# Optimization experiments

Hardware: AMD Instinct MI355X
Metric: run time of the kernel (lower is better)

The kernel has to match this reference:

```python
import jax, jax.numpy as jnp
from jax import lax
import numpy as np


def _qlayer(x, theta):
    """Simulate QLayer: RX(x_i) encoder + trainable RX(theta_i) per wire
    (they commute -> single RX(x_i+theta_i) on |0>), then ring of CNOTs,
    then <Z> on each wire.  x: (B, n) float, theta: (n,). Returns (B, n)."""
    B, n = x.shape
    a = x + theta[None, :]
    c = jnp.cos(a * 0.5)
    s = jnp.sin(a * 0.5)
    # RX(a)|0> = [cos(a/2), -i sin(a/2)] per wire -> product state
    amps = jnp.stack([c + 0j, -1j * s], axis=-1)  # (B, n, 2) complex64
    state = amps[:, 0]  # (B, 2)
    for w in range(1, n):
        state = state[..., None] * amps[:, w].reshape((B,) + (1,) * w + (2,))
    # state: (B, 2, 2, ..., 2), axis w+1 == wire w
    for ctrl in range(n):
        tgt = (ctrl + 1) % n
        s0 = jnp.take(state, 0, axis=ctrl + 1)   # control = 0 block
        s1 = jnp.take(state, 1, axis=ctrl + 1)   # control = 1 block
        t_ax = tgt + 1 if tgt < ctrl else tgt    # target axis after removing ctrl axis
        s1 = jnp.flip(s1, axis=t_ax)             # X on target
        state = jnp.stack([s0, s1], axis=ctrl + 1)
    p = state.real ** 2 + state.imag ** 2
    axes = tuple(range(1, n + 1))
    zs = []
    for w in range(n):
        other = tuple(ax for ax in axes if ax != w + 1)
        pw = jnp.sum(p, axis=other)              # (B, 2)
        zs.append(pw[:, 0] - pw[:, 1])           # <Z_w> = P(0) - P(1)
    return jnp.stack(zs, axis=1)


def setup_inputs() -> dict:
    key = jax.random.key(0)
    ks = jax.random.split(key, 13)
    T, B, D, NQ = 64, 256, 512, 6
    lim = 1.0 / np.sqrt(D + NQ)

    def lin(k):
        k1, k2 = jax.random.split(k)
        W = jax.random.uniform(k1, (D + NQ, NQ), jnp.float32, -lim, lim)
        b = jax.random.uniform(k2, (NQ,), jnp.float32, -lim, lim)
        return W, b

    Wf, bf = lin(ks[0]); Wi, bi = lin(ks[1]); Wu, bu = lin(ks[2]); Wo, bo = lin(ks[3])
    theta_f = jax.random.normal(ks[4], (NQ,), jnp.float32) * 0.1
    theta_i = jax.random.normal(ks[5], (NQ,), jnp.float32) * 0.1
    theta_u = jax.random.normal(ks[6], (NQ,), jnp.float32) * 0.1
    theta_o = jax.random.normal(ks[7], (NQ,), jnp.float32) * 0.1
    inputs = jax.random.normal(ks[8], (T, B, D), jnp.float32)
    return {"inputs": inputs,
            "Wf": Wf, "bf": bf, "Wi": Wi, "bi": bi,
            "Wu": Wu, "bu": bu, "Wo": Wo, "bo": bo,
            "theta_f": theta_f, "theta_i": theta_i,
            "theta_u": theta_u, "theta_o": theta_o}


def reference(inputs, Wf, bf, Wi, bi, Wu, bu, Wo, bo,
              theta_f, theta_i, theta_u, theta_o):
    B = inputs.shape[1]
    NQ = theta_f.shape[0]  # hidden_dim == n_qubits
    h0 = jnp.zeros((B, NQ), inputs.dtype)
    c0 = jnp.zeros((B, NQ), inputs.dtype)

    def step(carry, x):
        hx, cx = carry
        comb = jnp.concatenate([x, hx], axis=1)          # (B, D+NQ)
        f = jax.nn.sigmoid(_qlayer(comb @ Wf + bf, theta_f))
        i = jax.nn.sigmoid(_qlayer(comb @ Wi + bi, theta_i))
        g = jnp.tanh(_qlayer(comb @ Wu + bu, theta_u))
        o = jax.nn.sigmoid(_qlayer(comb @ Wo + bo, theta_o))
        cx2 = f * cx + i * g
        hx2 = o * jnp.tanh(cx2)
        return (hx2, cx2), hx2

    (hx, cx), outputs = lax.scan(step, (h0, c0), inputs)  # outputs: (T, B, NQ)
    return outputs, hx, cx
```

## Files before the change

kernel.cpp:

```cpp
#include <hip/hip_runtime.h>


typedef float v2f __attribute__((ext_vector_type(2)));

__device__ __forceinline__ float fast_rcp(float x) { return __builtin_amdgcn_rcpf(x); }

template <int CTRL>
__device__ __forceinline__ float dpp_add(float x) {
    int t = __builtin_amdgcn_mov_dpp(__float_as_int(x), CTRL, 0xF, 0xF, true);
    return x + __int_as_float(t);
}

template <int G>
__device__ __forceinline__ float quad_bcast(float v) {
    int i = __builtin_amdgcn_mov_dpp(__float_as_int(v), G * 0x55, 0xF, 0xF, true);
    return __int_as_float(i);
}

__global__ __launch_bounds__(512, 2) void gemm_pre(
    const float* __restrict__ X,
    const float* __restrict__ Wf, const float* __restrict__ bf,
    const float* __restrict__ Wi, const float* __restrict__ bi,
    const float* __restrict__ Wu, const float* __restrict__ bu,
    const float* __restrict__ Wo, const float* __restrict__ bo,
    const float* __restrict__ thf, const float* __restrict__ thi,
    const float* __restrict__ thu, const float* __restrict__ tho,
    float* __restrict__ pre)
{
    __shared__ float W_lds[13312];

    const int tid  = threadIdx.x;
    const int w    = tid >> 6;
    const int lane = tid & 63;
    const int rowbase = blockIdx.x * 64;

    #pragma unroll
    for (int i = 0; i < 4; ++i) {
        const float* Wp = (i==0)?Wf:(i==1)?Wi:(i==2)?Wu:Wo;
        int k = tid;
        const float2* s = (const float2*)(Wp + k*6);
        float2* d = (float2*)(W_lds + k*26 + i*6);
        d[0] = s[0]; d[1] = s[1]; d[2] = s[2];
    }
    __syncthreads();

    v2f acc[8][12];
    #pragma unroll
    for (int r = 0; r < 8; ++r)
        #pragma unroll
        for (int p = 0; p < 12; ++p) acc[r][p] = (v2f){0.f, 0.f};

    const float* Xr0 = X + (rowbase + w*8)*512 + lane;

    float pa[8];
    #pragma unroll
    for (int r = 0; r < 8; ++r) pa[r] = Xr0[r*512];

    #pragma unroll
    for (int kb = 0; kb < 512; kb += 64) {
        const v2f* wrow = (const v2f*)(W_lds + (kb + lane)*26);
        #pragma unroll
        for (int p = 0; p < 12; ++p) {
            v2f wv = wrow[p];
            #pragma unroll
            for (int r = 0; r < 8; ++r)
                acc[r][p] = __builtin_elementwise_fma((v2f){pa[r],pa[r]}, wv, acc[r][p]);
        }
        if (kb < 448) {
            #pragma unroll
            for (int r = 0; r < 8; ++r) pa[r] = Xr0[kb + 64 + r*512];
        }
    }

    #pragma unroll
    for (int r = 0; r < 8; ++r)
        #pragma unroll
        for (int p = 0; p < 12; ++p) {
            float x = acc[r][p].x;
            x = dpp_add<0xB1>(x);
            x = dpp_add<0x4E>(x);
            acc[r][p].x = x;
            float y = acc[r][p].y;
            y = dpp_add<0xB1>(y);
            y = dpp_add<0x4E>(y);
            acc[r][p].y = y;
        }

    #define ACCV(v) ((((v) & 1) == 0) ? acc[(v)/24][((v)%24)/2].x \
                                      : acc[(v)/24][((v)%24)/2].y)
    const int j = lane & 3;
    const int q = lane >> 2;
    const bool j1 = (j & 1) != 0, j2 = (j & 2) != 0;

    __syncthreads();

    #pragma unroll
    for (int pass = 0; pass < 2; ++pass) {
        if ((w >> 2) == pass) {
            const int w4 = w & 3;
            #pragma unroll
            for (int i = 0; i < 48; ++i) {
                float c0 = ACCV(i*4 + 0), c1 = ACCV(i*4 + 1);
                float c2 = ACCV(i*4 + 2), c3 = ACCV(i*4 + 3);
                float lo = j1 ? c1 : c0;
                float hi = j1 ? c3 : c2;
                float s  = j2 ? hi : lo;
                W_lds[(w4*192 + i*4 + j)*16 + q] = s;
            }
        }
        __syncthreads();
        for (int o = tid; o < 768; o += 512) {
            int wv4 = o / 192, v = o - wv4*192;
            int rr = v / 24, col = v - rr*24;
            const float4* rp = (const float4*)(W_lds + (wv4*192 + v)*16);
            float4 r0 = rp[0], r1 = rp[1], r2 = rp[2], r3 = rp[3];
            float s = ((r0.x+r0.y)+(r0.z+r0.w)) + ((r1.x+r1.y)+(r1.z+r1.w))
                    + ((r2.x+r2.y)+(r2.z+r2.w)) + ((r3.x+r3.y)+(r3.z+r3.w));
            int g = col / 6, jg = col - g*6;
            const float* bb = (g==0)?bf:(g==1)?bi:(g==2)?bu:bo;
            const float* tt = (g==0)?thf:(g==1)?thi:(g==2)?thu:tho;
            s += bb[jg] + tt[jg];
            int row = rowbase + (pass*4 + wv4)*8 + rr;
            pre[row*24 + col] = s;
        }
        __syncthreads();
    }
    #undef ACCV
}

__global__ __launch_bounds__(64, 1) void qlstm_scan(
    const float* __restrict__ pre,
    const float* __restrict__ Wf, const float* __restrict__ Wi,
    const float* __restrict__ Wu, const float* __restrict__ Wo,
    float* __restrict__ out)
{
    const int lane = threadIdx.x;
    const int bl   = lane >> 2;
    const int g    = lane & 3;
    const int b    = blockIdx.x * 16 + bl;

    const float* Wg = (g==0)?Wf:(g==1)?Wi:(g==2)?Wu:Wo;
    v2f Wh2[6][3];
    #pragma unroll
    for (int j = 0; j < 6; ++j)
        #pragma unroll
        for (int p = 0; p < 3; ++p)
            Wh2[j][p] = (v2f){Wg[(512 + j)*6 + 2*p], Wg[(512 + j)*6 + 2*p + 1]};

    const float k1 = (g==2) ? 2.f : 1.f;
    const float k2 = (g==2) ? 2.f : 1.f;
    const float k3 = (g==2) ? -1.f : 0.f;

    float h[6], c[6];
    #pragma unroll
    for (int w = 0; w < 6; ++w) { h[w] = 0.f; c[w] = 0.f; }

    const float* pb = pre + b*24 + g*6;
    v2f x0 = *(const v2f*)(pb);
    v2f x1 = *(const v2f*)(pb + 2);
    v2f x2 = *(const v2f*)(pb + 4);
    v2f n0 = *(const v2f*)(pb + 256*24);
    v2f n1 = *(const v2f*)(pb + 256*24 + 2);
    v2f n2 = *(const v2f*)(pb + 256*24 + 4);

    for (int t = 0; t < 64; ++t) {
        v2f a2[3] = {x0, x1, x2};
        x0 = n0; x1 = n1; x2 = n2;
        int tn = (t < 62) ? (t + 2) : 63;
        const float* pn = pre + (tn*256 + b)*24 + g*6;
        n0 = *(const v2f*)(pn);
        n1 = *(const v2f*)(pn + 2);
        n2 = *(const v2f*)(pn + 4);

        #pragma unroll
        for (int j = 0; j < 6; ++j) {
            v2f hj = (v2f){h[j], h[j]};
            #pragma unroll
            for (int p = 0; p < 3; ++p)
                a2[p] = __builtin_elementwise_fma(hj, Wh2[j][p], a2[p]);
        }

        float C[6];
        C[0] = __cosf(a2[0].x); C[1] = __cosf(a2[0].y);
        C[2] = __cosf(a2[1].x); C[3] = __cosf(a2[1].y);
        C[4] = __cosf(a2[2].x); C[5] = __cosf(a2[2].y);

        float p01 = C[0]*C[1], p23 = C[2]*C[3], p45 = C[4]*C[5];
        float z[6];
        z[1] = p01;
        z[2] = p01*C[2];
        z[3] = p01*p23;
        z[4] = z[3]*C[4];
        z[5] = z[3]*p45;
        z[0] = C[1]*(p23*p45);

        float act[6];
        #pragma unroll
        for (int w = 0; w < 6; ++w) {
            float e = __expf(-k1 * z[w]);
            act[w] = fmaf(k2, fast_rcp(1.f + e), k3);
        }

        float F[6], I[6], U[6], O[6];
        #pragma unroll
        for (int w = 0; w < 6; ++w) {
            F[w] = quad_bcast<0>(act[w]);
            I[w] = quad_bcast<1>(act[w]);
            U[w] = quad_bcast<2>(act[w]);
            O[w] = quad_bcast<3>(act[w]);
        }

        #pragma unroll
        for (int w = 0; w < 6; ++w) {
            c[w] = fmaf(F[w], c[w], I[w]*U[w]);
            float e  = __expf(-2.f * c[w]);
            float tc = fmaf(2.f, fast_rcp(1.f + e), -1.f);
            h[w] = O[w]*tc;
        }

        if (g < 3) {
            float2 v;
            v.x = (g==0) ? h[0] : (g==1) ? h[2] : h[4];
            v.y = (g==0) ? h[1] : (g==1) ? h[3] : h[5];
            *(float2*)(out + (t*256 + b)*6 + g*2) = v;
        }
    }

    if (g < 3) {
        float2 v;
        v.x = (g==0) ? h[0] : (g==1) ? h[2] : h[4];
        v.y = (g==0) ? h[1] : (g==1) ? h[3] : h[5];
        *(float2*)(out + 64*256*6 + b*6 + g*2) = v;
        float2 u;
        u.x = (g==0) ? c[0] : (g==1) ? c[2] : c[4];
        u.y = (g==0) ? c[1] : (g==1) ? c[3] : c[5];
        *(float2*)(out + 64*256*6 + 256*6 + b*6 + g*2) = u;
    }
}

extern "C" void kernel_launch(void* const* d_in, const int* in_sizes, int n_in,
                              void* d_out, int out_size, void* d_ws, size_t ws_size,
                              hipStream_t stream) {
    const float* X   = (const float*)d_in[0];
    const float* Wf  = (const float*)d_in[1];
    const float* bf_ = (const float*)d_in[2];
    const float* Wi  = (const float*)d_in[3];
    const float* bi_ = (const float*)d_in[4];
    const float* Wu  = (const float*)d_in[5];
    const float* bu_ = (const float*)d_in[6];
    const float* Wo  = (const float*)d_in[7];
    const float* bo_ = (const float*)d_in[8];
    const float* thf = (const float*)d_in[9];
    const float* thi = (const float*)d_in[10];
    const float* thu = (const float*)d_in[11];
    const float* tho = (const float*)d_in[12];

    float* pre = (float*)d_ws;
    float* out = (float*)d_out;

    gemm_pre<<<256, 512, 0, stream>>>(X, Wf, bf_, Wi, bi_, Wu, bu_, Wo, bo_,
                                      thf, thi, thu, tho, pre);
    qlstm_scan<<<16, 64, 0, stream>>>(pre, Wf, Wi, Wu, Wo, out);
}
```

Baseline: 144.9 us.

## Split GEMM columns across waves, double grid, and use rational sigmoid/tanh approximations

```diff
diff --git a/kernel.cpp b/kernel.cpp
--- a/kernel.cpp
+++ b/kernel.cpp
@@ -27,30 +27,37 @@
     const float* __restrict__ thu, const float* __restrict__ tho,
     float* __restrict__ pre)
 {
-    __shared__ float W_lds[13312];
+    __shared__ float W_lds[12800];
 
     const int tid  = threadIdx.x;
     const int w    = tid >> 6;
     const int lane = tid & 63;
-    const int rowbase = blockIdx.x * 64;
-
-    #pragma unroll
-    for (int i = 0; i < 4; ++i) {
-        const float* Wp = (i==0)?Wf:(i==1)?Wi:(i==2)?Wu:Wo;
-        int k = tid;
-        const float2* s = (const float2*)(Wp + k*6);
-        float2* d = (float2*)(W_lds + k*26 + i*6);
-        d[0] = s[0]; d[1] = s[1]; d[2] = s[2];
+    const int rg   = w >> 1;
+    const int cg   = w & 1;
+    const int rowbase = blockIdx.x * 32;
+
+    {
+        const int k = tid;
+        #pragma unroll
+        for (int g = 0; g < 4; ++g) {
+            const float* Wp = (g==0)?Wf:(g==1)?Wi:(g==2)?Wu:Wo;
+            const float2* s = (const float2*)(Wp + k*6);
+            float2 s0 = s[0], s1 = s[1], s2 = s[2];
+            float* d = W_lds + k*25 + g*6;
+            d[0] = s0.x; d[1] = s0.y; d[2] = s1.x;
+            d[3] = s1.y; d[4] = s2.x; d[5] = s2.y;
+        }
     }
     __syncthreads();
 
-    v2f acc[8][12];
+    v2f acc[8][6];
     #pragma unroll
     for (int r = 0; r < 8; ++r)
         #pragma unroll
-        for (int p = 0; p < 12; ++p) acc[r][p] = (v2f){0.f, 0.f};
-
-    const float* Xr0 = X + (rowbase + w*8)*512 + lane;
+        for (int p = 0; p < 6; ++p) acc[r][p] = (v2f){0.f, 0.f};
+
+    const float* Xr0 = X + (rowbase + rg*8)*512 + lane;
+    const int colbase = cg*12;
 
     float pa[8];
     #pragma unroll
@@ -58,10 +65,12 @@
 
     #pragma unroll
     for (int kb = 0; kb < 512; kb += 64) {
-        const v2f* wrow = (const v2f*)(W_lds + (kb + lane)*26);
-        #pragma unroll
-        for (int p = 0; p < 12; ++p) {
-            v2f wv = wrow[p];
+        const float* Wrow = W_lds + (kb + lane)*25 + colbase;
+        #pragma unroll
+        for (int p = 0; p < 6; ++p) {
+            float wa = Wrow[p];
+            float wb = Wrow[p + 6];
+            v2f wv = (v2f){wa, wb};
             #pragma unroll
             for (int r = 0; r < 8; ++r)
                 acc[r][p] = __builtin_elementwise_fma((v2f){pa[r],pa[r]}, wv, acc[r][p]);
@@ -75,7 +84,7 @@
     #pragma unroll
     for (int r = 0; r < 8; ++r)
         #pragma unroll
-        for (int p = 0; p < 12; ++p) {
+        for (int p = 0; p < 6; ++p) {
             float x = acc[r][p].x;
             x = dpp_add<0xB1>(x);
             x = dpp_add<0x4E>(x);
@@ -86,46 +95,44 @@
             acc[r][p].y = y;
         }
 
-    #define ACCV(v) ((((v) & 1) == 0) ? acc[(v)/24][((v)%24)/2].x \
-                                      : acc[(v)/24][((v)%24)/2].y)
+    #define ACCV(v) ((((v) % 12) < 6) ? acc[(v)/12][(v)%6].x \
+                                      : acc[(v)/12][(v)%6].y)
     const int j = lane & 3;
     const int q = lane >> 2;
     const bool j1 = (j & 1) != 0, j2 = (j & 2) != 0;
+    float sel[24];
+    #pragma unroll
+    for (int i = 0; i < 24; ++i) {
+        float c0 = ACCV(i*4 + 0), c1 = ACCV(i*4 + 1);
+        float c2 = ACCV(i*4 + 2), c3 = ACCV(i*4 + 3);
+        float lo = j1 ? c1 : c0;
+        float hi = j1 ? c3 : c2;
+        sel[i] = j2 ? hi : lo;
+    }
+    #undef ACCV
 
     __syncthreads();
-
-    #pragma unroll
-    for (int pass = 0; pass < 2; ++pass) {
-        if ((w >> 2) == pass) {
-            const int w4 = w & 3;
-            #pragma unroll
-            for (int i = 0; i < 48; ++i) {
-                float c0 = ACCV(i*4 + 0), c1 = ACCV(i*4 + 1);
-                float c2 = ACCV(i*4 + 2), c3 = ACCV(i*4 + 3);
-                float lo = j1 ? c1 : c0;
-                float hi = j1 ? c3 : c2;
-                float s  = j2 ? hi : lo;
-                W_lds[(w4*192 + i*4 + j)*16 + q] = s;
-            }
-        }
-        __syncthreads();
-        for (int o = tid; o < 768; o += 512) {
-            int wv4 = o / 192, v = o - wv4*192;
-            int rr = v / 24, col = v - rr*24;
-            const float4* rp = (const float4*)(W_lds + (wv4*192 + v)*16);
-            float4 r0 = rp[0], r1 = rp[1], r2 = rp[2], r3 = rp[3];
-            float s = ((r0.x+r0.y)+(r0.z+r0.w)) + ((r1.x+r1.y)+(r1.z+r1.w))
-                    + ((r2.x+r2.y)+(r2.z+r2.w)) + ((r3.x+r3.y)+(r3.z+r3.w));
-            int g = col / 6, jg = col - g*6;
-            const float* bb = (g==0)?bf:(g==1)?bi:(g==2)?bu:bo;
-            const float* tt = (g==0)?thf:(g==1)?thi:(g==2)?thu:tho;
-            s += bb[jg] + tt[jg];
-            int row = rowbase + (pass*4 + wv4)*8 + rr;
-            pre[row*24 + col] = s;
-        }
-        __syncthreads();
-    }
-    #undef ACCV
+    #pragma unroll
+    for (int i = 0; i < 24; ++i) {
+        W_lds[(w*96 + i*4 + j)*16 + q] = sel[i];
+    }
+    __syncthreads();
+
+    for (int o = tid; o < 768; o += 512) {
+        int ww = o / 96, v = o - ww*96;
+        int rr = v / 12, ph = v - rr*12;
+        const float4* rp = (const float4*)(W_lds + (ww*96 + v)*16);
+        float4 r0 = rp[0], r1 = rp[1], r2 = rp[2], r3 = rp[3];
+        float s = ((r0.x+r0.y)+(r0.z+r0.w)) + ((r1.x+r1.y)+(r1.z+r1.w))
+                + ((r2.x+r2.y)+(r2.z+r2.w)) + ((r3.x+r3.y)+(r3.z+r3.w));
+        int col = (ww & 1)*12 + ph;
+        int g = col / 6, jg = col - g*6;
+        const float* bb = (g==0)?bf:(g==1)?bi:(g==2)?bu:bo;
+        const float* tt = (g==0)?thf:(g==1)?thi:(g==2)?thu:tho;
+        s += bb[jg] + tt[jg];
+        int row = rowbase + (ww >> 1)*8 + rr;
+        pre[row*24 + col] = s;
+    }
 }
 
 __global__ __launch_bounds__(64, 1) void qlstm_scan(
@@ -147,9 +154,12 @@
         for (int p = 0; p < 3; ++p)
             Wh2[j][p] = (v2f){Wg[(512 + j)*6 + 2*p], Wg[(512 + j)*6 + 2*p + 1]};
 
-    const float k1 = (g==2) ? 2.f : 1.f;
-    const float k2 = (g==2) ? 2.f : 1.f;
-    const float k3 = (g==2) ? -1.f : 0.f;
+    const float c0 = (g==2) ? 0.f        : 0.5f;
+    const float n0 = (g==2) ? 15.f       : 0.25f;
+    const float n1 = (g==2) ? 1.f        : -0.020833333f;
+    const float n2 = (g==2) ? 0.f        : 0.0020833333f;
+    const float d0 = (g==2) ? 15.f       : 1.f;
+    const float d1 = (g==2) ? 6.f        : 0.f;
 
     float h[6], c[6];
     #pragma unroll
@@ -159,18 +169,18 @@
     v2f x0 = *(const v2f*)(pb);
     v2f x1 = *(const v2f*)(pb + 2);
     v2f x2 = *(const v2f*)(pb + 4);
-    v2f n0 = *(const v2f*)(pb + 256*24);
-    v2f n1 = *(const v2f*)(pb + 256*24 + 2);
-    v2f n2 = *(const v2f*)(pb + 256*24 + 4);
+    v2f n0v = *(const v2f*)(pb + 256*24);
+    v2f n1v = *(const v2f*)(pb + 256*24 + 2);
+    v2f n2v = *(const v2f*)(pb + 256*24 + 4);
 
     for (int t = 0; t < 64; ++t) {
         v2f a2[3] = {x0, x1, x2};
-        x0 = n0; x1 = n1; x2 = n2;
+        x0 = n0v; x1 = n1v; x2 = n2v;
         int tn = (t < 62) ? (t + 2) : 63;
         const float* pn = pre + (tn*256 + b)*24 + g*6;
-        n0 = *(const v2f*)(pn);
-        n1 = *(const v2f*)(pn + 2);
-        n2 = *(const v2f*)(pn + 4);
+        n0v = *(const v2f*)(pn);
+        n1v = *(const v2f*)(pn + 2);
+        n2v = *(const v2f*)(pn + 4);
 
         #pragma unroll
         for (int j = 0; j < 6; ++j) {
@@ -197,8 +207,10 @@
         float act[6];
         #pragma unroll
         for (int w = 0; w < 6; ++w) {
-            float e = __expf(-k1 * z[w]);
-            act[w] = fmaf(k2, fast_rcp(1.f + e), k3);
+            float y   = z[w]*z[w];
+            float num = fmaf(y, fmaf(y, n2, n1), n0);
+            float den = fmaf(y, d1, d0);
+            act[w] = fmaf(z[w]*num, fast_rcp(den), c0);
         }
 
         float F[6], I[6], U[6], O[6];
@@ -213,8 +225,10 @@
         #pragma unroll
         for (int w = 0; w < 6; ++w) {
             c[w] = fmaf(F[w], c[w], I[w]*U[w]);
-            float e  = __expf(-2.f * c[w]);
-            float tc = fmaf(2.f, fast_rcp(1.f + e), -1.f);
+            float y   = c[w]*c[w];
+            float num = fmaf(y, fmaf(y, 1.f, 105.f), 945.f);
+            float den = fmaf(y, fmaf(y, 15.f, 420.f), 945.f);
+            float tc  = c[w]*num*fast_rcp(den);
             h[w] = O[w]*tc;
         }
 
@@ -258,7 +272,7 @@
     float* pre = (float*)d_ws;
     float* out = (float*)d_out;
 
-    gemm_pre<<<256, 512, 0, stream>>>(X, Wf, bf_, Wi, bi_, Wu, bu_, Wo, bo_,
+    gemm_pre<<<512, 512, 0, stream>>>(X, Wf, bf_, Wi, bi_, Wu, bu_, Wo, bo_,
                                       thf, thi, thu, tho, pre);
     qlstm_scan<<<16, 64, 0, stream>>>(pre, Wf, Wi, Wu, Wo, out);
 }
```

Result: faster. 139.5 us (-3.7%).
